# Performance work log

Measured on AMD Instinct MI355X. Metric: run time of the kernel, lower is better.

## Reference

```python
import jax, jax.numpy as jnp
import numpy as np

B = 16384
STATE = 524   # state_dim / output_size
IENC = 256    # INet output dim
ZD = 32       # z_dim
H = 256       # expert hidden size
E = 5         # num_experts
HG = 256      # gating hidden size
IN1 = STATE + IENC + ZD   # 812, PredictionNet layer-1 input
IN2 = H + ZD              # 288, layers 2/3 input


def _uni(k, shape):
    # matches PredictionNet.init_params glorot-style uniform bound
    bound = float(np.sqrt(6.0 / (shape[-2] * shape[-1])))
    return jax.random.uniform(k, shape, jnp.float32, -bound, bound)


def setup_inputs() -> dict:
    key = jax.random.key(0)
    ks = jax.random.split(key, 12)
    d = {}
    d['z'] = jax.random.normal(ks[0], (B, ZD), jnp.float32)
    d['p_prev'] = jax.random.normal(ks[1], (B, STATE), jnp.float32)
    d['I'] = jax.random.normal(ks[2], (B, 2048), jnp.float32)
    # gating network: (state+z) -> HG -> HG//2 -> E
    d['gw1'] = _uni(ks[3], (STATE + ZD, HG)); d['gb1'] = jnp.zeros((HG,), jnp.float32)
    d['gw2'] = _uni(ks[4], (HG, HG // 2));    d['gb2'] = jnp.zeros((HG // 2,), jnp.float32)
    d['gw3'] = _uni(ks[5], (HG // 2, E));     d['gb3'] = jnp.zeros((E,), jnp.float32)
    # INet: 2048 -> 256 -> 256 -> 256
    d['iw1'] = _uni(ks[6], (2048, IENC)); d['ib1'] = jnp.zeros((IENC,), jnp.float32)
    d['iw2'] = _uni(ks[7], (IENC, IENC)); d['ib2'] = jnp.zeros((IENC,), jnp.float32)
    d['iw3'] = _uni(ks[8], (IENC, IENC)); d['ib3'] = jnp.zeros((IENC,), jnp.float32)
    # expert weights [E, in, out], biases [E, out]
    d['w_l1'] = _uni(ks[9], (E, IN1, H));     d['b_l1'] = jnp.zeros((E, H), jnp.float32)
    d['w_l2'] = _uni(ks[10], (E, IN2, H));    d['b_l2'] = jnp.zeros((E, H), jnp.float32)
    d['w_l3'] = _uni(ks[11], (E, IN2, STATE)); d['b_l3'] = jnp.zeros((E, STATE), jnp.float32)
    return d


def reference(z, p_prev, I, gw1, gb1, gw2, gb2, gw3, gb3,
              iw1, ib1, iw2, ib2, iw3, ib3,
              w_l1, b_l1, w_l2, b_l2, w_l3, b_l3):
    elu = jax.nn.elu
    # gating network -> softmax blending coefficients omega [B, E]
    g = elu(jnp.concatenate([z, p_prev], axis=1) @ gw1 + gb1)
    g = elu(g @ gw2 + gb2)
    omega = jax.nn.softmax(g @ gw3 + gb3, axis=-1)
    # interaction encoder
    Ienc = elu(elu(elu(I @ iw1 + ib1) @ iw2 + ib2) @ iw3 + ib3)
    x = jnp.concatenate([p_prev, Ienc], axis=1)  # [B, STATE+IENC]

    def moe_linear(h, W, b):
        # same math as sum_e omega_e * (h @ W_e) + omega @ b, without
        # materializing per-sample blended [B, in, out] weights
        per_expert = jnp.einsum('bi,eio->beo', h, W)
        return jnp.einsum('be,beo->bo', omega, per_expert) + omega @ b

    h0 = jnp.concatenate([z, x], axis=1)          # [B, 812]
    h1 = elu(moe_linear(h0, w_l1, b_l1))          # [B, 256]
    h2 = elu(moe_linear(jnp.concatenate([z, h1], axis=1), w_l2, b_l2))
    h3 = moe_linear(jnp.concatenate([z, h2], axis=1), w_l3, b_l3)  # [B, 524]
    return h3
```

## Files before the change

kernel.cpp:

```cpp
#include <hip/hip_runtime.h>
#include <hip/hip_bf16.h>
#include <cstdint>
#include <cstddef>


#define BATCH 16384

typedef __attribute__((ext_vector_type(8))) short short8;
typedef __attribute__((ext_vector_type(4))) float f32x4;
typedef unsigned short u16;
typedef unsigned int u32;

typedef __attribute__((address_space(3))) void lds_t;
typedef __attribute__((address_space(1))) void gmem_t;

__device__ __forceinline__ void gload16(const u16* g, u16* l) {
  __builtin_amdgcn_global_load_lds((gmem_t*)(u16*)g, (lds_t*)l, 16, 0, 0);
}

__device__ __forceinline__ void barrier_nodrain() {
  asm volatile("" ::: "memory");
  __builtin_amdgcn_s_barrier();
  asm volatile("" ::: "memory");
}
__device__ __forceinline__ void barrier_lds() {
  asm volatile("s_waitcnt lgkmcnt(0)" ::: "memory");
  __builtin_amdgcn_s_barrier();
  asm volatile("" ::: "memory");
}

__device__ __forceinline__ float bf2f(u16 u) {
  union { float f; u32 i; } v; v.i = ((u32)u) << 16; return v.f;
}
__device__ __forceinline__ u16 f2bf(float f) {
  union { float f; u32 i; } v; v.f = f;
  u32 x = v.i;
  return (u16)((x + 0x7fffu + ((x >> 16) & 1u)) >> 16);
}
__device__ __forceinline__ u16 load_bf(const void* p, long i, int f32) {
  return f32 ? f2bf(((const float*)p)[i]) : ((const u16*)p)[i];
}
__device__ __forceinline__ float elu_f(float x) { return x > 0.f ? x : expm1f(x); }

__device__ __forceinline__ int swz(int row, int q) { return q ^ ((row >> 1) & 3); }

struct TPSeg { long end; int K, N, Kp, Np; };

__global__ __launch_bounds__(256) void prep_all(
    const void* __restrict__ z, const void* __restrict__ p,
    const void* __restrict__ I, int* __restrict__ flagp,
    u16* __restrict__ h0, u16* __restrict__ h1c, u16* __restrict__ h2c,
    u16* __restrict__ Ibf,
    const void* ib1, const void* ib2, const void* ib3,
    const void* gb1, const void* gb2, const void* gb3,
    const void* gw3, const void* bl1, const void* bl2, const void* bl3,
    u16* __restrict__ smallc,
    const void* s0, const void* s1, const void* s2, const void* s3,
    const void* s4, const void* s5, const void* s6, const void* s7,
    u16* d0, u16* d1, u16* d2, u16* d3, u16* d4, u16* d5, u16* d6, u16* d7)
{
  __shared__ int scnt[4];
  {
    u32 w = ((const u32*)z)[threadIdx.x];
    int e = (w >> 7) & 0xFF;
    unsigned long long m = __ballot(e >= 112 && e <= 142);
    if ((threadIdx.x & 63) == 0) scnt[threadIdx.x >> 6] = __popcll(m);
  }
  __syncthreads();
  const int f32 = (scnt[0] + scnt[1] + scnt[2] + scnt[3] < 128) ? 1 : 0;
  if (blockIdx.x == 0 && threadIdx.x == 0) *flagp = f32;

  if (blockIdx.x == 0) {
    for (long j = threadIdx.x; j < 7100; j += 256) {
      u16 v;
      if      (j < 256)  v = load_bf(ib1, j,        f32);
      else if (j < 512)  v = load_bf(ib2, j - 256,  f32);
      else if (j < 768)  v = load_bf(ib3, j - 512,  f32);
      else if (j < 1024) v = load_bf(gb1, j - 768,  f32);
      else if (j < 1152) v = load_bf(gb2, j - 1024, f32);
      else if (j < 1280) v = (j - 1152 < 5) ? load_bf(gb3, j - 1152, f32) : (u16)0;
      else if (j < 1920) v = load_bf(gw3, j - 1280, f32);
      else if (j < 3200) v = load_bf(bl1, j - 1920, f32);
      else if (j < 4480) v = load_bf(bl2, j - 3200, f32);
      else               v = load_bf(bl3, j - 4480, f32);
      smallc[j] = v;
    }
  }

  const TPSeg seg[8] = {
    {  524288, 2048, 256, 2048, 256 },
    {  589824,  256, 256,  256, 256 },
    {  655360,  256, 256,  256, 256 },
    {  802816,  556, 256,  576, 256 },
    {  835584,  256, 128,  256, 128 },
    { 1900544,  812, 256,  832, 256 },
    { 2269184,  288, 256,  288, 256 },
    { 3098624,  288, 524,  288, 576 },
  };
  const void* const srcs[8] = { s0, s1, s2, s3, s4, s5, s6, s7 };
  u16* const dsts[8] = { d0, d1, d2, d3, d4, d5, d6, d7 };

  const long NC = (long)BATCH * 2048 / 8;
  const long NP = (long)BATCH * 208;
  const long NT = 774656;
  const long total = NC + NP + NT;
  const long stride = (long)gridDim.x * blockDim.x;

  for (long it = (long)blockIdx.x * 256 + threadIdx.x; it < total; it += stride) {
    if (it < NC) {
      const long t = it;
      if (f32) {
        const float4* src = (const float4*)I;
        float4 a = src[t * 2], b = src[t * 2 + 1];
        union { u16 r[8]; uint4 v; } u;
        u.r[0] = f2bf(a.x); u.r[1] = f2bf(a.y); u.r[2] = f2bf(a.z); u.r[3] = f2bf(a.w);
        u.r[4] = f2bf(b.x); u.r[5] = f2bf(b.y); u.r[6] = f2bf(b.z); u.r[7] = f2bf(b.w);
        *(uint4*)(Ibf + t * 8) = u.v;
      } else {
        *(uint4*)(Ibf + t * 8) = ((const uint4*)I)[t];
      }
    } else if (it < NC + NP) {
      const long j = it - NC;
      const int b = (int)(j / 208);
      const int c = (int)(j % 208) * 4;
      ushort4 v;
      if (c < 32) {
        const long zi = (long)b * 32 + c;
        if (f32) {
          const float4 f = *(const float4*)((const float*)z + zi);
          v.x = f2bf(f.x); v.y = f2bf(f.y); v.z = f2bf(f.z); v.w = f2bf(f.w);
        } else {
          v = *(const ushort4*)((const u16*)z + zi);
        }
        *(ushort4*)(h0 + (long)b * 832 + c) = v;
        *(ushort4*)(h1c + (long)b * 288 + c) = v;
        *(ushort4*)(h2c + (long)b * 288 + c) = v;
      } else if (c < 556) {
        const long pi = (long)b * 524 + (c - 32);
        if (f32) {
          const float4 f = *(const float4*)((const float*)p + pi);
          v.x = f2bf(f.x); v.y = f2bf(f.y); v.z = f2bf(f.z); v.w = f2bf(f.w);
        } else {
          v = *(const ushort4*)((const u16*)p + pi);
        }
        *(ushort4*)(h0 + (long)b * 832 + c) = v;
      } else {
        v.x = 0; v.y = 0; v.z = 0; v.w = 0;
        *(ushort4*)(h0 + (long)b * 832 + c) = v;
      }
    } else {
      const long jd = (it - NC - NP) * 4;
      int s = 0; long sbase = 0;
      while (jd >= seg[s].end) { sbase = seg[s].end; ++s; }
      const long jj = jd - sbase;
      const int Kp = seg[s].Kp, Np = seg[s].Np, Kk = seg[s].K, Nn = seg[s].N;
      const int k = (int)(jj % Kp);
      const long tt = jj / Kp;
      const int n = (int)(tt % Np);
      const int e = (int)(tt / Np);
      ushort4 v; v.x = 0; v.y = 0; v.z = 0; v.w = 0;
      if (k < Kk && n < Nn) {
        const long sb = (long)e * Kk * Nn + (long)k * Nn + n;
        v.x = load_bf(srcs[s], sb, f32);
        v.y = load_bf(srcs[s], sb + Nn, f32);
        v.z = load_bf(srcs[s], sb + 2 * (long)Nn, f32);
        v.w = load_bf(srcs[s], sb + 3 * (long)Nn, f32);
      }
      *(ushort4*)(dsts[s] + jj) = v;
    }
  }
}

struct GemmDesc {
  const u16* A; const u16* Wt; const u16* bias; u16* C;
  int lda, ldw, ldc, col_off, K, ny;
};

__global__ __launch_bounds__(256, 2) void gemm64m(GemmDesc da, GemmDesc db)
{
  __shared__ __align__(16) u16 sA[3][64 * 32];
  __shared__ __align__(16) u16 sB[3][128 * 32];

  int bn = blockIdx.y;
  GemmDesc d;
  if (bn < da.ny) { d = da; } else { bn -= da.ny; d = db; }

  const int tid  = threadIdx.x;
  const int bm   = blockIdx.x;
  const int lane = tid & 63, wave = tid >> 6;
  const int wm = (wave & 1) * 32, wn = (wave >> 1) * 64;
  const int lrow = lane & 15, lq = lane >> 4;

  const int sq    = (lane & 3) ^ ((lane >> 3) & 3);
  const int srowA = 16 * wave + (lane >> 2);
  const int srowB = 32 * wave + (lane >> 2);
  const u16* Ag = d.A  + (size_t)(bm * 64  + srowA) * d.lda + sq * 8;
  const u16* Wg = d.Wt + (size_t)(bn * 128 + srowB) * d.ldw + sq * 8;
  const int laOff = wave * 512;
  const int lbOff = wave * 1024;
  const int ldw = d.ldw;

  f32x4 acc[2][4] = {};
  const int nt = d.K / 32;

  gload16(Ag, sA[0] + laOff);
  gload16(Wg, sB[0] + lbOff);
  gload16(Wg + (size_t)16 * ldw, sB[0] + lbOff + 512);
  gload16(Ag + 32, sA[1] + laOff);
  gload16(Wg + 32, sB[1] + lbOff);
  gload16(Wg + (size_t)16 * ldw + 32, sB[1] + lbOff + 512);

  for (int t = 0; t < nt; ++t) {
    const int cur = t % 3;
    barrier_nodrain();
    if (t + 2 < nt) {
      const int nb = (t + 2) % 3;
      const int k0 = (t + 2) * 32;
      gload16(Ag + k0, sA[nb] + laOff);
      gload16(Wg + k0, sB[nb] + lbOff);
      gload16(Wg + (size_t)16 * ldw + k0, sB[nb] + lbOff + 512);
    }
    const int ahead = nt - 1 - t;
    if (ahead >= 2)      asm volatile("s_waitcnt vmcnt(6)" ::: "memory");
    else if (ahead == 1) asm volatile("s_waitcnt vmcnt(3)" ::: "memory");
    else                 asm volatile("s_waitcnt vmcnt(0)" ::: "memory");
    barrier_nodrain();

    short8 a[2], b[4];
#pragma unroll
    for (int i = 0; i < 2; ++i) {
      const int r = wm + i * 16 + lrow;
      a[i] = *(const short8*)(sA[cur] + r * 32 + swz(r, lq) * 8);
    }
#pragma unroll
    for (int i = 0; i < 4; ++i) {
      const int r = wn + i * 16 + lrow;
      b[i] = *(const short8*)(sB[cur] + r * 32 + swz(r, lq) * 8);
    }

    __builtin_amdgcn_s_setprio(1);
#pragma unroll
    for (int mi = 0; mi < 2; ++mi)
#pragma unroll
      for (int ni = 0; ni < 4; ++ni)
        acc[mi][ni] = __builtin_amdgcn_mfma_f32_16x16x32_bf16(a[mi], b[ni], acc[mi][ni], 0, 0, 0);
    __builtin_amdgcn_s_setprio(0);
  }

#pragma unroll
  for (int ni = 0; ni < 4; ++ni) {
    const int col = bn * 128 + wn + ni * 16 + lrow;
    const float bv = bf2f(d.bias[col]);
#pragma unroll
    for (int mi = 0; mi < 2; ++mi) {
#pragma unroll
      for (int r = 0; r < 4; ++r) {
        const int row = bm * 64 + wm + mi * 16 + lq * 4 + r;
        float v = acc[mi][ni][r] + bv;
        v = elu_f(v);
        d.C[(size_t)row * d.ldc + d.col_off + col] = f2bf(v);
      }
    }
  }
}

template<bool ELU>
__global__ __launch_bounds__(256, 2) void moe_gemm(
    const u16* __restrict__ A, int lda,
    const u16* __restrict__ Wt, int ldw, long wstride_e,
    const u16* __restrict__ bias, int bias_n,
    const u16* __restrict__ g2, const u16* __restrict__ gw3c,
    const u16* __restrict__ gb3c,
    void* __restrict__ C, int ldc, int col_off, int n_store, int K,
    const int* __restrict__ flagp, int is_final)
{
  __shared__ __align__(16) u16 sA[2][128 * 32];
  __shared__ __align__(16) u16 sW[2][5 * 64 * 32];
  __shared__ float som[128 * 5];
  __shared__ float sbias[5][64];
  __shared__ float sgw[128 * 5];
  __shared__ float sgb[5];

  const int tid  = threadIdx.x;
  const int bm   = blockIdx.x, bn = blockIdx.y;
  const int lane = tid & 63, wave = tid >> 6;
  const int wm = (wave & 1) * 64, wn = (wave >> 1) * 32;
  const int lrow = lane & 15, lq = lane >> 4;
  const int f32out = is_final ? *flagp : 0;

  const int sq = (lane & 3) ^ ((lane >> 3) & 3);
  const int srowA = 32 * wave + (lane >> 2);
  const int srowW = 16 * wave + (lane >> 2);
  const u16* Ag = A  + (size_t)(bm * 128 + srowA) * lda + sq * 8;
  const u16* Wg = Wt + (size_t)(bn * 64 + srowW) * ldw + sq * 8;
  const int laOff = wave * 1024;
  const int lWoff = wave * 512;

  auto stage = [&](int buf, int k0) {
    gload16(Ag + k0, sA[buf] + laOff);
    gload16(Ag + (size_t)16 * lda + k0, sA[buf] + laOff + 512);
#pragma unroll
    for (int e = 0; e < 5; ++e)
      gload16(Wg + e * wstride_e + k0, sW[buf] + e * 2048 + lWoff);
  };

  f32x4 acc[5][4][2] = {};
  const int nt = K / 32;

  stage(0, 0);
  for (int t2 = tid; t2 < 960; t2 += 256) {
    if (t2 < 640) {
      sgw[t2] = bf2f(gw3c[t2]);
    } else {
      const int j = t2 - 640;
      const int e = j >> 6, c = j & 63;
      const int col = bn * 64 + c;
      sbias[e][c] = (col < bias_n) ? bf2f(bias[(size_t)e * bias_n + col]) : 0.f;
    }
  }
  if (tid < 5) sgb[tid] = bf2f(gb3c[tid]);
  barrier_lds();
  if (tid < 128) {
    const u16* gr = g2 + (size_t)(bm * 128 + tid) * 128;
    float t[5];
#pragma unroll
    for (int e = 0; e < 5; ++e) t[e] = sgb[e];
    for (int k = 0; k < 128; k += 2) {
      const u32 gp = *(const u32*)(gr + k);
      const float x0 = bf2f((u16)(gp & 0xffffu));
      const float x1 = bf2f((u16)(gp >> 16));
#pragma unroll
      for (int e = 0; e < 5; ++e)
        t[e] += x0 * sgw[k * 5 + e] + x1 * sgw[(k + 1) * 5 + e];
    }
    float m = t[0];
#pragma unroll
    for (int e = 1; e < 5; ++e) m = fmaxf(m, t[e]);
    float ssum = 0.f;
#pragma unroll
    for (int e = 0; e < 5; ++e) { t[e] = expf(t[e] - m); ssum += t[e]; }
    const float inv = 1.f / ssum;
#pragma unroll
    for (int e = 0; e < 5; ++e) som[tid * 5 + e] = t[e] * inv;
  }

  for (int t = 0; t < nt; ++t) {
    const int cur = t & 1;
    barrier_nodrain();
    if (t + 1 < nt) {
      stage(cur ^ 1, (t + 1) * 32);
      asm volatile("s_waitcnt vmcnt(7)" ::: "memory");
    } else {
      asm volatile("s_waitcnt vmcnt(0)" ::: "memory");
    }
    barrier_nodrain();

    short8 a[4];
#pragma unroll
    for (int i = 0; i < 4; ++i) {
      const int r = wm + i * 16 + lrow;
      a[i] = *(const short8*)(sA[cur] + r * 32 + swz(r, lq) * 8);
    }
    const int rb0 = wn + lrow, rb1 = rb0 + 16;
    const int ob0 = rb0 * 32 + swz(rb0, lq) * 8;
    const int ob1 = rb1 * 32 + swz(rb1, lq) * 8;
    __builtin_amdgcn_s_setprio(1);
#pragma unroll
    for (int e = 0; e < 5; ++e) {
      short8 b0 = *(const short8*)(sW[cur] + e * 2048 + ob0);
      short8 b1 = *(const short8*)(sW[cur] + e * 2048 + ob1);
#pragma unroll
      for (int mi = 0; mi < 4; ++mi) {
        acc[e][mi][0] = __builtin_amdgcn_mfma_f32_16x16x32_bf16(a[mi], b0, acc[e][mi][0], 0, 0, 0);
        acc[e][mi][1] = __builtin_amdgcn_mfma_f32_16x16x32_bf16(a[mi], b1, acc[e][mi][1], 0, 0, 0);
      }
    }
    __builtin_amdgcn_s_setprio(0);
  }

#pragma unroll
  for (int mi = 0; mi < 4; ++mi) {
#pragma unroll
    for (int r = 0; r < 4; ++r) {
      const int rl = wm + mi * 16 + lq * 4 + r;
      const int row = bm * 128 + rl;
      float om[5];
#pragma unroll
      for (int e = 0; e < 5; ++e) om[e] = som[rl * 5 + e];
#pragma unroll
      for (int ni = 0; ni < 2; ++ni) {
        const int c = wn + ni * 16 + lrow;
        const int col = bn * 64 + c;
        if (col < n_store) {
          float v = 0.f;
#pragma unroll
          for (int e = 0; e < 5; ++e) v += om[e] * (acc[e][mi][ni][r] + sbias[e][c]);
          if (ELU) v = elu_f(v);
          const size_t idx = (size_t)row * ldc + col_off + col;
          if (f32out) ((float*)C)[idx] = v;
          else        ((u16*)C)[idx]   = f2bf(v);
        }
      }
    }
  }
}

extern "C" void kernel_launch(void* const* d_in, const int* in_sizes, int n_in,
                              void* d_out, int out_size, void* d_ws, size_t ws_size,
                              hipStream_t stream)
{
  const void* z    = d_in[0];
  const void* pprev= d_in[1];
  const void* I    = d_in[2];
  const void* gw1  = d_in[3];
  const void* gb1  = d_in[4];
  const void* gw2  = d_in[5];
  const void* gb2  = d_in[6];
  const void* gw3  = d_in[7];
  const void* gb3  = d_in[8];
  const void* iw1  = d_in[9];
  const void* ib1  = d_in[10];
  const void* iw2  = d_in[11];
  const void* ib2  = d_in[12];
  const void* iw3  = d_in[13];
  const void* ib3  = d_in[14];
  const void* wl1  = d_in[15];
  const void* bl1  = d_in[16];
  const void* wl2  = d_in[17];
  const void* bl2  = d_in[18];
  const void* wl3  = d_in[19];
  const void* bl3  = d_in[20];

  char* base = (char*)d_ws;
  size_t off = 0;
  auto alloc = [&](size_t bytes) -> void* {
    void* p = base + off;
    off = (off + bytes + 255) & ~(size_t)255;
    return p;
  };

  const size_t B = BATCH;
  int* flagp   = (int*)alloc(256);
  u16* h0      = (u16*)alloc(B * 832 * 2);
  u16* h1c     = (u16*)alloc(B * 288 * 2);
  u16* h2c     = (u16*)alloc(B * 288 * 2);
  u16* i1      = (u16*)alloc(B * 256 * 2);
  u16* i2      = (u16*)alloc(B * 256 * 2);
  u16* g1      = (u16*)alloc(B * 256 * 2);
  u16* g2      = (u16*)alloc(B * 128 * 2);
  u16* Ibf     = (u16*)alloc(B * 2048 * 2);
  u16* smallc  = (u16*)alloc(7100 * 2);
  u16* iw1t = (u16*)alloc((size_t)256 * 2048 * 2);
  u16* iw2t = (u16*)alloc((size_t)256 * 256 * 2);
  u16* iw3t = (u16*)alloc((size_t)256 * 256 * 2);
  u16* gw1t = (u16*)alloc((size_t)256 * 576 * 2);
  u16* gw2t = (u16*)alloc((size_t)128 * 256 * 2);
  u16* wl1t = (u16*)alloc((size_t)5 * 256 * 832 * 2);
  u16* wl2t = (u16*)alloc((size_t)5 * 256 * 288 * 2);
  u16* wl3t = (u16*)alloc((size_t)5 * 576 * 288 * 2);
  (void)in_sizes; (void)n_in; (void)out_size; (void)ws_size;

  u16* ib1c = smallc + 0,   *ib2c = smallc + 256, *ib3c = smallc + 512;
  u16* gb1c = smallc + 768, *gb2c = smallc + 1024, *gb3c = smallc + 1152;
  u16* gw3c = smallc + 1280;
  u16* bl1c = smallc + 1920, *bl2c = smallc + 3200, *bl3c = smallc + 4480;

  prep_all<<<2048, 256, 0, stream>>>(z, pprev, I, flagp, h0, h1c, h2c, Ibf,
      ib1, ib2, ib3, gb1, gb2, gb3, gw3, bl1, bl2, bl3, smallc,
      iw1, iw2, iw3, gw1, gw2, wl1, wl2, wl3,
      iw1t, iw2t, iw3t, gw1t, gw2t, wl1t, wl2t, wl3t);

  GemmDesc inet1 = { Ibf, iw1t, ib1c, i1, 2048, 2048, 256, 0,   2048, 2 };
  GemmDesc gat1  = { h0,  gw1t, gb1c, g1,  832,  576, 256, 0,    576, 2 };
  GemmDesc inet2 = { i1,  iw2t, ib2c, i2,  256,  256, 256, 0,    256, 2 };
  GemmDesc gat2  = { g1,  gw2t, gb2c, g2,  256,  256, 128, 0,    256, 1 };
  GemmDesc inet3 = { i2,  iw3t, ib3c, h0,  256,  256, 832, 556,  256, 2 };

  gemm64m<<<dim3(BATCH/64, 4), 256, 0, stream>>>(inet1, gat1);
  gemm64m<<<dim3(BATCH/64, 3), 256, 0, stream>>>(inet2, gat2);
  gemm64m<<<dim3(BATCH/64, 2), 256, 0, stream>>>(inet3, inet3);

  moe_gemm<true><<<dim3(BATCH/128, 4), 256, 0, stream>>>(
      h0, 832, wl1t, 832, (long)256 * 832, bl1c, 256, g2, gw3c, gb3c,
      h1c, 288, 32, 256, 832, flagp, 0);
  moe_gemm<true><<<dim3(BATCH/128, 4), 256, 0, stream>>>(
      h1c, 288, wl2t, 288, (long)256 * 288, bl2c, 256, g2, gw3c, gb3c,
      h2c, 288, 32, 256, 288, flagp, 0);
  moe_gemm<false><<<dim3(BATCH/128, 9), 256, 0, stream>>>(
      h2c, 288, wl3t, 288, (long)576 * 288, bl3c, 524, g2, gw3c, gb3c,
      d_out, 524, 0, 524, 288, flagp, 1);
}
```

Baseline: 515.1 us.

## Fuse fp32-to-bf16 conversion of I into INet GEMM, widen tiles to full N

Stops the prep kernel from converting the 16384x2048 input I to a bf16 workspace copy. The first INet GEMM now reads I directly through registers, converts it and writes the A tile to LDS. The dense GEMM tile widens from 128 to 256 columns so each block covers the whole N, which means A is read only once. The gw2 weights are padded to 256 columns and a store mask handles the 128-wide layer. The prep copy of p_prev/z also moves to 8-element vectors. The costs are more registers and LDS per block, fewer blocks per GEMM, and a missing barrier_lds definition if it is not in the hidden lines.

```diff
diff --git a/kernel.cpp b/kernel.cpp
--- a/kernel.cpp
+++ b/kernel.cpp
@@ -48,9 +48,8 @@
 
 __global__ __launch_bounds__(256) void prep_all(
     const void* __restrict__ z, const void* __restrict__ p,
-    const void* __restrict__ I, int* __restrict__ flagp,
+    int* __restrict__ flagp,
     u16* __restrict__ h0, u16* __restrict__ h1c, u16* __restrict__ h2c,
-    u16* __restrict__ Ibf,
     const void* ib1, const void* ib2, const void* ib3,
     const void* gb1, const void* gb2, const void* gb3,
     const void* gw3, const void* bl1, const void* bl2, const void* bl3,
@@ -92,64 +91,68 @@
     {  589824,  256, 256,  256, 256 },
     {  655360,  256, 256,  256, 256 },
     {  802816,  556, 256,  576, 256 },
-    {  835584,  256, 128,  256, 128 },
-    { 1900544,  812, 256,  832, 256 },
-    { 2269184,  288, 256,  288, 256 },
-    { 3098624,  288, 524,  288, 576 },
+    {  868352,  256, 128,  256, 256 },
+    { 1933312,  812, 256,  832, 256 },
+    { 2301952,  288, 256,  288, 256 },
+    { 3131392,  288, 524,  288, 576 },
   };
   const void* const srcs[8] = { s0, s1, s2, s3, s4, s5, s6, s7 };
   u16* const dsts[8] = { d0, d1, d2, d3, d4, d5, d6, d7 };
 
-  const long NC = (long)BATCH * 2048 / 8;
-  const long NP = (long)BATCH * 208;
-  const long NT = 774656;
-  const long total = NC + NP + NT;
+  const long NP = (long)BATCH * 104;
+  const long NT = 3131392 / 4;
+  const long total = NP + NT;
   const long stride = (long)gridDim.x * blockDim.x;
 
   for (long it = (long)blockIdx.x * 256 + threadIdx.x; it < total; it += stride) {
-    if (it < NC) {
-      const long t = it;
-      if (f32) {
-        const float4* src = (const float4*)I;
-        float4 a = src[t * 2], b = src[t * 2 + 1];
-        union { u16 r[8]; uint4 v; } u;
-        u.r[0] = f2bf(a.x); u.r[1] = f2bf(a.y); u.r[2] = f2bf(a.z); u.r[3] = f2bf(a.w);
-        u.r[4] = f2bf(b.x); u.r[5] = f2bf(b.y); u.r[6] = f2bf(b.z); u.r[7] = f2bf(b.w);
-        *(uint4*)(Ibf + t * 8) = u.v;
-      } else {
-        *(uint4*)(Ibf + t * 8) = ((const uint4*)I)[t];
+    if (it < NP) {
+      const int b = (int)(it / 104);
+      const int c = (int)(it % 104) * 8;
+      uint4 w; w.x = 0; w.y = 0; w.z = 0; w.w = 0;
+      if (c < 32) {
+        if (f32) {
+          const float4 f0 = *(const float4*)((const float*)z + (long)b * 32 + c);
+          const float4 f1 = *(const float4*)((const float*)z + (long)b * 32 + c + 4);
+          w.x = (u32)f2bf(f0.x) | ((u32)f2bf(f0.y) << 16);
+          w.y = (u32)f2bf(f0.z) | ((u32)f2bf(f0.w) << 16);
+          w.z = (u32)f2bf(f1.x) | ((u32)f2bf(f1.y) << 16);
+          w.w = (u32)f2bf(f1.z) | ((u32)f2bf(f1.w) << 16);
+        } else {
+          w = *(const uint4*)((const u16*)z + (long)b * 32 + c);
+        }
+        *(uint4*)(h0 + (long)b * 832 + c) = w;
+        *(uint4*)(h1c + (long)b * 288 + c) = w;
+        *(uint4*)(h2c + (long)b * 288 + c) = w;
+        continue;
       }
-    } else if (it < NC + NP) {
-      const long j = it - NC;
-      const int b = (int)(j / 208);
-      const int c = (int)(j % 208) * 4;
-      ushort4 v;
-      if (c < 32) {
-        const long zi = (long)b * 32 + c;
-        if (f32) {
-          const float4 f = *(const float4*)((const float*)z + zi);
-          v.x = f2bf(f.x); v.y = f2bf(f.y); v.z = f2bf(f.z); v.w = f2bf(f.w);
-        } else {
-          v = *(const ushort4*)((const u16*)z + zi);
-        }
-        *(ushort4*)(h0 + (long)b * 832 + c) = v;
-        *(ushort4*)(h1c + (long)b * 288 + c) = v;
-        *(ushort4*)(h2c + (long)b * 288 + c) = v;
-      } else if (c < 556) {
+      if (c < 552) {
         const long pi = (long)b * 524 + (c - 32);
         if (f32) {
-          const float4 f = *(const float4*)((const float*)p + pi);
-          v.x = f2bf(f.x); v.y = f2bf(f.y); v.z = f2bf(f.z); v.w = f2bf(f.w);
+          const float4 f0 = *(const float4*)((const float*)p + pi);
+          const float4 f1 = *(const float4*)((const float*)p + pi + 4);
+          w.x = (u32)f2bf(f0.x) | ((u32)f2bf(f0.y) << 16);
+          w.y = (u32)f2bf(f0.z) | ((u32)f2bf(f0.w) << 16);
+          w.z = (u32)f2bf(f1.x) | ((u32)f2bf(f1.y) << 16);
+          w.w = (u32)f2bf(f1.z) | ((u32)f2bf(f1.w) << 16);
         } else {
-          v = *(const ushort4*)((const u16*)p + pi);
+          const uint2 a0 = *(const uint2*)((const u16*)p + pi);
+          const uint2 a1 = *(const uint2*)((const u16*)p + pi + 4);
+          w.x = a0.x; w.y = a0.y; w.z = a1.x; w.w = a1.y;
         }
-        *(ushort4*)(h0 + (long)b * 832 + c) = v;
-      } else {
-        v.x = 0; v.y = 0; v.z = 0; v.w = 0;
-        *(ushort4*)(h0 + (long)b * 832 + c) = v;
+      } else if (c == 552) {
+        const long pi = (long)b * 524 + 520;
+        if (f32) {
+          const float4 f0 = *(const float4*)((const float*)p + pi);
+          w.x = (u32)f2bf(f0.x) | ((u32)f2bf(f0.y) << 16);
+          w.y = (u32)f2bf(f0.z) | ((u32)f2bf(f0.w) << 16);
+        } else {
+          const uint2 a0 = *(const uint2*)((const u16*)p + pi);
+          w.x = a0.x; w.y = a0.y;
+        }
       }
+      *(uint4*)(h0 + (long)b * 832 + c) = w;
     } else {
-      const long jd = (it - NC - NP) * 4;
+      const long jd = (it - NP) * 4;
       int s = 0; long sbase = 0;
       while (jd >= seg[s].end) { sbase = seg[s].end; ++s; }
       const long jj = jd - sbase;
@@ -172,93 +175,129 @@
 }
 
 struct GemmDesc {
-  const u16* A; const u16* Wt; const u16* bias; u16* C;
-  int lda, ldw, ldc, col_off, K, ny;
+  const void* A; const u16* Wt; const u16* bias; u16* C;
+  int lda, ldw, ldc, col_off, K, n_store, a_mode;
 };
 
-__global__ __launch_bounds__(256, 2) void gemm64m(GemmDesc da, GemmDesc db)
+__global__ __launch_bounds__(256, 2) void gemm64n(GemmDesc da, GemmDesc db,
+                                                  const int* __restrict__ flagp)
 {
-  __shared__ __align__(16) u16 sA[3][64 * 32];
-  __shared__ __align__(16) u16 sB[3][128 * 32];
-
-  int bn = blockIdx.y;
-  GemmDesc d;
-  if (bn < da.ny) { d = da; } else { bn -= da.ny; d = db; }
+  __shared__ __align__(16) u16 sAf[3 * 64 * 32];
+  __shared__ __align__(16) u16 sBf[3 * 256 * 32];
+
+  const GemmDesc d = blockIdx.y ? db : da;
+  const int f32A = d.a_mode ? *flagp : 0;
 
   const int tid  = threadIdx.x;
   const int bm   = blockIdx.x;
   const int lane = tid & 63, wave = tid >> 6;
-  const int wm = (wave & 1) * 32, wn = (wave >> 1) * 64;
+  const int wm = (wave & 1) * 32, wn = (wave >> 1) * 128;
   const int lrow = lane & 15, lq = lane >> 4;
 
   const int sq    = (lane & 3) ^ ((lane >> 3) & 3);
   const int srowA = 16 * wave + (lane >> 2);
-  const int srowB = 32 * wave + (lane >> 2);
-  const u16* Ag = d.A  + (size_t)(bm * 64  + srowA) * d.lda + sq * 8;
-  const u16* Wg = d.Wt + (size_t)(bn * 128 + srowB) * d.ldw + sq * 8;
+  const size_t abase = (size_t)(bm * 64 + srowA) * d.lda + sq * 8;
+  const float* Af = (const float*)d.A;
+  const u16*   Ab = (const u16*)d.A;
   const int laOff = wave * 512;
-  const int lbOff = wave * 1024;
+
   const int ldw = d.ldw;
-
-  f32x4 acc[2][4] = {};
+  const int srB = (lane >> 2);
+  const u16* Wg0 = d.Wt + (size_t)(64 * wave +  0 + srB) * ldw + sq * 8;
+  const u16* Wg1 = d.Wt + (size_t)(64 * wave + 16 + srB) * ldw + sq * 8;
+  const u16* Wg2 = d.Wt + (size_t)(64 * wave + 32 + srB) * ldw + sq * 8;
+  const u16* Wg3 = d.Wt + (size_t)(64 * wave + 48 + srB) * ldw + sq * 8;
+  const int lb0 = wave * 2048, lb1 = lb0 + 512, lb2 = lb0 + 1024, lb3 = lb0 + 1536;
+
+  float4 fA[2][2];
+  uint2  uA[2][2];
+  f32x4 acc[2][8] = {};
   const int nt = d.K / 32;
 
-  gload16(Ag, sA[0] + laOff);
-  gload16(Wg, sB[0] + lbOff);
-  gload16(Wg + (size_t)16 * ldw, sB[0] + lbOff + 512);
-  gload16(Ag + 32, sA[1] + laOff);
-  gload16(Wg + 32, sB[1] + lbOff);
-  gload16(Wg + (size_t)16 * ldw + 32, sB[1] + lbOff + 512);
-
-  for (int t = 0; t < nt; ++t) {
-    const int cur = t % 3;
-    barrier_nodrain();
-    if (t + 2 < nt) {
-      const int nb = (t + 2) % 3;
-      const int k0 = (t + 2) * 32;
-      gload16(Ag + k0, sA[nb] + laOff);
-      gload16(Wg + k0, sB[nb] + lbOff);
-      gload16(Wg + (size_t)16 * ldw + k0, sB[nb] + lbOff + 512);
-    }
-    const int ahead = nt - 1 - t;
-    if (ahead >= 2)      asm volatile("s_waitcnt vmcnt(6)" ::: "memory");
-    else if (ahead == 1) asm volatile("s_waitcnt vmcnt(3)" ::: "memory");
-    else                 asm volatile("s_waitcnt vmcnt(0)" ::: "memory");
-    barrier_nodrain();
-
-    short8 a[2], b[4];
-#pragma unroll
-    for (int i = 0; i < 2; ++i) {
-      const int r = wm + i * 16 + lrow;
-      a[i] = *(const short8*)(sA[cur] + r * 32 + swz(r, lq) * 8);
-    }
-#pragma unroll
-    for (int i = 0; i < 4; ++i) {
-      const int r = wn + i * 16 + lrow;
-      b[i] = *(const short8*)(sB[cur] + r * 32 + swz(r, lq) * 8);
-    }
-
-    __builtin_amdgcn_s_setprio(1);
-#pragma unroll
-    for (int mi = 0; mi < 2; ++mi)
-#pragma unroll
-      for (int ni = 0; ni < 4; ++ni)
-        acc[mi][ni] = __builtin_amdgcn_mfma_f32_16x16x32_bf16(a[mi], b[ni], acc[mi][ni], 0, 0, 0);
-    __builtin_amdgcn_s_setprio(0);
-  }
-
-#pragma unroll
-  for (int ni = 0; ni < 4; ++ni) {
-    const int col = bn * 128 + wn + ni * 16 + lrow;
-    const float bv = bf2f(d.bias[col]);
-#pragma unroll
-    for (int mi = 0; mi < 2; ++mi) {
-#pragma unroll
-      for (int r = 0; r < 4; ++r) {
-        const int row = bm * 64 + wm + mi * 16 + lq * 4 + r;
-        float v = acc[mi][ni][r] + bv;
-        v = elu_f(v);
-        d.C[(size_t)row * d.ldc + d.col_off + col] = f2bf(v);
+#define STAGE_LOAD(SET, k0_)                                          \
+  { const int k0s = (k0_);                                            \
+    if (f32A) {                                                       \
+      fA[SET][0] = *(const float4*)(Af + abase + k0s);                \
+      fA[SET][1] = *(const float4*)(Af + abase + k0s + 4);            \
+    } else {                                                          \
+      uA[SET][0] = *(const uint2*)(Ab + abase + k0s);                 \
+      uA[SET][1] = *(const uint2*)(Ab + abase + k0s + 4);             \
+    }                                                                 \
+    u16* sBb = sBf + ((k0s >> 5) % 3) * 8192;                         \
+    gload16(Wg0 + k0s, sBb + lb0);                                    \
+    gload16(Wg1 + k0s, sBb + lb1);                                    \
+    gload16(Wg2 + k0s, sBb + lb2);                                    \
+    gload16(Wg3 + k0s, sBb + lb3); }
+
+#define AWRITE(SET, bi_)                                              \
+  { uint4 wv;                                                         \
+    if (f32A) {                                                       \
+      wv.x = (u32)f2bf(fA[SET][0].x) | ((u32)f2bf(fA[SET][0].y) << 16); \
+      wv.y = (u32)f2bf(fA[SET][0].z) | ((u32)f2bf(fA[SET][0].w) << 16); \
+      wv.z = (u32)f2bf(fA[SET][1].x) | ((u32)f2bf(fA[SET][1].y) << 16); \
+      wv.w = (u32)f2bf(fA[SET][1].z) | ((u32)f2bf(fA[SET][1].w) << 16); \
+    } else {                                                          \
+      wv.x = uA[SET][0].x; wv.y = uA[SET][0].y;                       \
+      wv.z = uA[SET][1].x; wv.w = uA[SET][1].y;                       \
+    }                                                                 \
+    *(uint4*)(sAf + (bi_) * 2048 + laOff + lane * 8) = wv; }
+
+#define GSTEP(T, S, SO)                                               \
+  { barrier_lds();                                                    \
+    if ((T) + 2 < nt) STAGE_LOAD(S, ((T) + 2) * 32);                  \
+    const int ahead = nt - 1 - (T);                                   \
+    if (ahead >= 2)      asm volatile("s_waitcnt vmcnt(10)" ::: "memory"); \
+    else if (ahead == 1) asm volatile("s_waitcnt vmcnt(4)"  ::: "memory"); \
+    else                 asm volatile("s_waitcnt vmcnt(0)"  ::: "memory"); \
+    if ((T) + 1 < nt) AWRITE(SO, ((T) + 1) % 3);                      \
+    barrier_nodrain();                                                \
+    const int cb = (T) % 3;                                           \
+    short8 a[2], b[8];                                                \
+    _Pragma("unroll")                                                 \
+    for (int i = 0; i < 2; ++i) {                                     \
+      const int r = wm + i * 16 + lrow;                               \
+      a[i] = *(const short8*)(sAf + cb * 2048 + r * 32 + swz(r, lq) * 8); \
+    }                                                                 \
+    _Pragma("unroll")                                                 \
+    for (int i = 0; i < 8; ++i) {                                     \
+      const int r = wn + i * 16 + lrow;                               \
+      b[i] = *(const short8*)(sBf + cb * 8192 + r * 32 + swz(r, lq) * 8); \
+    }                                                                 \
+    __builtin_amdgcn_s_setprio(1);                                    \
+    _Pragma("unroll")                                                 \
+    for (int mi = 0; mi < 2; ++mi)                                    \
+      _Pragma("unroll")                                               \
+      for (int ni = 0; ni < 8; ++ni)                                  \
+        acc[mi][ni] = __builtin_amdgcn_mfma_f32_16x16x32_bf16(a[mi], b[ni], acc[mi][ni], 0, 0, 0); \
+    __builtin_amdgcn_s_setprio(0); }
+
+  STAGE_LOAD(0, 0)
+  STAGE_LOAD(1, 32)
+  asm volatile("s_waitcnt vmcnt(10)" ::: "memory");
+  AWRITE(0, 0)
+
+  for (int t = 0; t < nt; t += 2) {
+    GSTEP(t, 0, 1)
+    GSTEP(t + 1, 1, 0)
+  }
+#undef GSTEP
+#undef AWRITE
+#undef STAGE_LOAD
+
+#pragma unroll
+  for (int ni = 0; ni < 8; ++ni) {
+    const int col = wn + ni * 16 + lrow;
+    if (col < d.n_store) {
+      const float bv = bf2f(d.bias[col]);
+#pragma unroll
+      for (int mi = 0; mi < 2; ++mi) {
+#pragma unroll
+        for (int r = 0; r < 4; ++r) {
+          const int row = bm * 64 + wm + mi * 16 + lq * 4 + r;
+          float v = acc[mi][ni][r] + bv;
+          v = elu_f(v);
+          d.C[(size_t)row * d.ldc + d.col_off + col] = f2bf(v);
+        }
       }
     }
   }
@@ -448,13 +487,12 @@
   u16* i2      = (u16*)alloc(B * 256 * 2);
   u16* g1      = (u16*)alloc(B * 256 * 2);
   u16* g2      = (u16*)alloc(B * 128 * 2);
-  u16* Ibf     = (u16*)alloc(B * 2048 * 2);
   u16* smallc  = (u16*)alloc(7100 * 2);
   u16* iw1t = (u16*)alloc((size_t)256 * 2048 * 2);
   u16* iw2t = (u16*)alloc((size_t)256 * 256 * 2);
   u16* iw3t = (u16*)alloc((size_t)256 * 256 * 2);
   u16* gw1t = (u16*)alloc((size_t)256 * 576 * 2);
-  u16* gw2t = (u16*)alloc((size_t)128 * 256 * 2);
+  u16* gw2t = (u16*)alloc((size_t)256 * 256 * 2);
   u16* wl1t = (u16*)alloc((size_t)5 * 256 * 832 * 2);
   u16* wl2t = (u16*)alloc((size_t)5 * 256 * 288 * 2);
   u16* wl3t = (u16*)alloc((size_t)5 * 576 * 288 * 2);
@@ -465,20 +503,20 @@
   u16* gw3c = smallc + 1280;
   u16* bl1c = smallc + 1920, *bl2c = smallc + 3200, *bl3c = smallc + 4480;
 
-  prep_all<<<2048, 256, 0, stream>>>(z, pprev, I, flagp, h0, h1c, h2c, Ibf,
+  prep_all<<<2048, 256, 0, stream>>>(z, pprev, flagp, h0, h1c, h2c,
       ib1, ib2, ib3, gb1, gb2, gb3, gw3, bl1, bl2, bl3, smallc,
       iw1, iw2, iw3, gw1, gw2, wl1, wl2, wl3,
       iw1t, iw2t, iw3t, gw1t, gw2t, wl1t, wl2t, wl3t);
 
-  GemmDesc inet1 = { Ibf, iw1t, ib1c, i1, 2048, 2048, 256, 0,   2048, 2 };
-  GemmDesc gat1  = { h0,  gw1t, gb1c, g1,  832,  576, 256, 0,    576, 2 };
-  GemmDesc inet2 = { i1,  iw2t, ib2c, i2,  256,  256, 256, 0,    256, 2 };
-  GemmDesc gat2  = { g1,  gw2t, gb2c, g2,  256,  256, 128, 0,    256, 1 };
-  GemmDesc inet3 = { i2,  iw3t, ib3c, h0,  256,  256, 832, 556,  256, 2 };
-
-  gemm64m<<<dim3(BATCH/64, 4), 256, 0, stream>>>(inet1, gat1);
-  gemm64m<<<dim3(BATCH/64, 3), 256, 0, stream>>>(inet2, gat2);
-  gemm64m<<<dim3(BATCH/64, 2), 256, 0, stream>>>(inet3, inet3);
+  GemmDesc inet1 = { I,   iw1t, ib1c, i1, 2048, 2048, 256, 0,   2048, 256, 1 };
+  GemmDesc gat1  = { h0,  gw1t, gb1c, g1,  832,  576, 256, 0,    576, 256, 0 };
+  GemmDesc inet2 = { i1,  iw2t, ib2c, i2,  256,  256, 256, 0,    256, 256, 0 };
+  GemmDesc gat2  = { g1,  gw2t, gb2c, g2,  256,  256, 128, 0,    256, 128, 0 };
+  GemmDesc inet3 = { i2,  iw3t, ib3c, h0,  256,  256, 832, 556,  256, 256, 0 };
+
+  gemm64n<<<dim3(BATCH/64, 2), 256, 0, stream>>>(inet1, gat1, flagp);
+  gemm64n<<<dim3(BATCH/64, 2), 256, 0, stream>>>(inet2, gat2, flagp);
+  gemm64n<<<dim3(BATCH/64, 1), 256, 0, stream>>>(inet3, inet3, flagp);
 
   moe_gemm<true><<<dim3(BATCH/128, 4), 256, 0, stream>>>(
       h0, 832, wl1t, 832, (long)256 * 832, bl1c, 256, g2, gw3c, gb3c,
```

After: 530.3 us. 1.03x slower.

## Skip bf16 copy of I when input is bf16, widen prep stores, raise occupancy

Applied to the files above, without the earlier changes.

When the inputs are already bf16, the prep kernel no longer copies I into a staging buffer. The first GEMM instead reads I directly, chosen through a runtime flag and an alternate A pointer. The p_prev/z packing loop now handles 8 elements per thread with 16-byte stores, and the GEMM launch bounds request 4 blocks per CU instead of 2. In the common fp32-input case only the wider prep stores and the occupancy change apply, and the higher occupancy target may force register spills.

```diff
diff --git a/kernel.cpp b/kernel.cpp
--- a/kernel.cpp
+++ b/kernel.cpp
@@ -101,53 +101,69 @@
   u16* const dsts[8] = { d0, d1, d2, d3, d4, d5, d6, d7 };
 
   const long NC = (long)BATCH * 2048 / 8;
-  const long NP = (long)BATCH * 208;
-  const long NT = 774656;
+  const long NP = (long)BATCH * 104;
+  const long NT = 3098624 / 4;
   const long total = NC + NP + NT;
   const long stride = (long)gridDim.x * blockDim.x;
 
   for (long it = (long)blockIdx.x * 256 + threadIdx.x; it < total; it += stride) {
     if (it < NC) {
-      const long t = it;
       if (f32) {
+        const long t = it;
         const float4* src = (const float4*)I;
         float4 a = src[t * 2], b = src[t * 2 + 1];
         union { u16 r[8]; uint4 v; } u;
         u.r[0] = f2bf(a.x); u.r[1] = f2bf(a.y); u.r[2] = f2bf(a.z); u.r[3] = f2bf(a.w);
         u.r[4] = f2bf(b.x); u.r[5] = f2bf(b.y); u.r[6] = f2bf(b.z); u.r[7] = f2bf(b.w);
         *(uint4*)(Ibf + t * 8) = u.v;
-      } else {
-        *(uint4*)(Ibf + t * 8) = ((const uint4*)I)[t];
       }
     } else if (it < NC + NP) {
       const long j = it - NC;
-      const int b = (int)(j / 208);
-      const int c = (int)(j % 208) * 4;
-      ushort4 v;
+      const int b = (int)(j / 104);
+      const int c = (int)(j % 104) * 8;
+      uint4 w; w.x = 0; w.y = 0; w.z = 0; w.w = 0;
       if (c < 32) {
-        const long zi = (long)b * 32 + c;
         if (f32) {
-          const float4 f = *(const float4*)((const float*)z + zi);
-          v.x = f2bf(f.x); v.y = f2bf(f.y); v.z = f2bf(f.z); v.w = f2bf(f.w);
+          const float4 f0 = *(const float4*)((const float*)z + (long)b * 32 + c);
+          const float4 f1 = *(const float4*)((const float*)z + (long)b * 32 + c + 4);
+          w.x = (u32)f2bf(f0.x) | ((u32)f2bf(f0.y) << 16);
+          w.y = (u32)f2bf(f0.z) | ((u32)f2bf(f0.w) << 16);
+          w.z = (u32)f2bf(f1.x) | ((u32)f2bf(f1.y) << 16);
+          w.w = (u32)f2bf(f1.z) | ((u32)f2bf(f1.w) << 16);
         } else {
-          v = *(const ushort4*)((const u16*)z + zi);
+          w = *(const uint4*)((const u16*)z + (long)b * 32 + c);
         }
-        *(ushort4*)(h0 + (long)b * 832 + c) = v;
-        *(ushort4*)(h1c + (long)b * 288 + c) = v;
-        *(ushort4*)(h2c + (long)b * 288 + c) = v;
-      } else if (c < 556) {
+        *(uint4*)(h0 + (long)b * 832 + c) = w;
+        *(uint4*)(h1c + (long)b * 288 + c) = w;
+        *(uint4*)(h2c + (long)b * 288 + c) = w;
+        continue;
+      }
+      if (c < 552) {
         const long pi = (long)b * 524 + (c - 32);
         if (f32) {
-          const float4 f = *(const float4*)((const float*)p + pi);
-          v.x = f2bf(f.x); v.y = f2bf(f.y); v.z = f2bf(f.z); v.w = f2bf(f.w);
+          const float4 f0 = *(const float4*)((const float*)p + pi);
+          const float4 f1 = *(const float4*)((const float*)p + pi + 4);
+          w.x = (u32)f2bf(f0.x) | ((u32)f2bf(f0.y) << 16);
+          w.y = (u32)f2bf(f0.z) | ((u32)f2bf(f0.w) << 16);
+          w.z = (u32)f2bf(f1.x) | ((u32)f2bf(f1.y) << 16);
+          w.w = (u32)f2bf(f1.z) | ((u32)f2bf(f1.w) << 16);
         } else {
-          v = *(const ushort4*)((const u16*)p + pi);
+          const uint2 a0 = *(const uint2*)((const u16*)p + pi);
+          const uint2 a1 = *(const uint2*)((const u16*)p + pi + 4);
+          w.x = a0.x; w.y = a0.y; w.z = a1.x; w.w = a1.y;
         }
-        *(ushort4*)(h0 + (long)b * 832 + c) = v;
-      } else {
-        v.x = 0; v.y = 0; v.z = 0; v.w = 0;
-        *(ushort4*)(h0 + (long)b * 832 + c) = v;
-      }
+      } else if (c == 552) {
+        const long pi = (long)b * 524 + 520;
+        if (f32) {
+          const float4 f0 = *(const float4*)((const float*)p + pi);
+          w.x = (u32)f2bf(f0.x) | ((u32)f2bf(f0.y) << 16);
+          w.y = (u32)f2bf(f0.z) | ((u32)f2bf(f0.w) << 16);
+        } else {
+          const uint2 a0 = *(const uint2*)((const u16*)p + pi);
+          w.x = a0.x; w.y = a0.y;
+        }
+      }
+      *(uint4*)(h0 + (long)b * 832 + c) = w;
     } else {
       const long jd = (it - NC - NP) * 4;
       int s = 0; long sbase = 0;
@@ -172,11 +188,12 @@
 }
 
 struct GemmDesc {
-  const u16* A; const u16* Wt; const u16* bias; u16* C;
-  int lda, ldw, ldc, col_off, K, ny;
+  const u16* A; const u16* Aalt; const u16* Wt; const u16* bias; u16* C;
+  int lda, ldw, ldc, col_off, K, ny, a_mode;
 };
 
-__global__ __launch_bounds__(256, 2) void gemm64m(GemmDesc da, GemmDesc db)
+__global__ __launch_bounds__(256, 4) void gemm64m(GemmDesc da, GemmDesc db,
+                                                  const int* __restrict__ flagp)
 {
   __shared__ __align__(16) u16 sA[3][64 * 32];
   __shared__ __align__(16) u16 sB[3][128 * 32];
@@ -184,6 +201,7 @@
   int bn = blockIdx.y;
   GemmDesc d;
   if (bn < da.ny) { d = da; } else { bn -= da.ny; d = db; }
+  const u16* Abase = (d.a_mode && *flagp) ? d.Aalt : d.A;
 
   const int tid  = threadIdx.x;
   const int bm   = blockIdx.x;
@@ -194,8 +212,8 @@
   const int sq    = (lane & 3) ^ ((lane >> 3) & 3);
   const int srowA = 16 * wave + (lane >> 2);
   const int srowB = 32 * wave + (lane >> 2);
-  const u16* Ag = d.A  + (size_t)(bm * 64  + srowA) * d.lda + sq * 8;
-  const u16* Wg = d.Wt + (size_t)(bn * 128 + srowB) * d.ldw + sq * 8;
+  const u16* Ag = Abase + (size_t)(bm * 64  + srowA) * d.lda + sq * 8;
+  const u16* Wg = d.Wt  + (size_t)(bn * 128 + srowB) * d.ldw + sq * 8;
   const int laOff = wave * 512;
   const int lbOff = wave * 1024;
   const int ldw = d.ldw;
@@ -470,15 +488,15 @@
       iw1, iw2, iw3, gw1, gw2, wl1, wl2, wl3,
       iw1t, iw2t, iw3t, gw1t, gw2t, wl1t, wl2t, wl3t);
 
-  GemmDesc inet1 = { Ibf, iw1t, ib1c, i1, 2048, 2048, 256, 0,   2048, 2 };
-  GemmDesc gat1  = { h0,  gw1t, gb1c, g1,  832,  576, 256, 0,    576, 2 };
-  GemmDesc inet2 = { i1,  iw2t, ib2c, i2,  256,  256, 256, 0,    256, 2 };
-  GemmDesc gat2  = { g1,  gw2t, gb2c, g2,  256,  256, 128, 0,    256, 1 };
-  GemmDesc inet3 = { i2,  iw3t, ib3c, h0,  256,  256, 832, 556,  256, 2 };
-
-  gemm64m<<<dim3(BATCH/64, 4), 256, 0, stream>>>(inet1, gat1);
-  gemm64m<<<dim3(BATCH/64, 3), 256, 0, stream>>>(inet2, gat2);
-  gemm64m<<<dim3(BATCH/64, 2), 256, 0, stream>>>(inet3, inet3);
+  GemmDesc inet1 = { (const u16*)I, Ibf, iw1t, ib1c, i1, 2048, 2048, 256, 0,   2048, 2, 1 };
+  GemmDesc gat1  = { h0, h0, gw1t, gb1c, g1,  832,  576, 256, 0,    576, 2, 0 };
+  GemmDesc inet2 = { i1, i1, iw2t, ib2c, i2,  256,  256, 256, 0,    256, 2, 0 };
+  GemmDesc gat2  = { g1, g1, gw2t, gb2c, g2,  256,  256, 128, 0,    256, 1, 0 };
+  GemmDesc inet3 = { i2, i2, iw3t, ib3c, h0,  256,  256, 832, 556,  256, 2, 0 };
+
+  gemm64m<<<dim3(BATCH/64, 4), 256, 0, stream>>>(inet1, gat1, flagp);
+  gemm64m<<<dim3(BATCH/64, 3), 256, 0, stream>>>(inet2, gat2, flagp);
+  gemm64m<<<dim3(BATCH/64, 2), 256, 0, stream>>>(inet3, inet3, flagp);
 
   moe_gemm<true><<<dim3(BATCH/128, 4), 256, 0, stream>>>(
       h0, 832, wl1t, 832, (long)256 * 832, bl1c, 256, g2, gw3c, gb3c,
```

New measurement: 517.1 us. About the same (+0.4%).
